# Kernel tuning notes

Measured on AMD Instinct MI355X. Metric: run time of the kernel, lower is better.

The kernel has to match this reference:

```python
import jax, jax.numpy as jnp
import numpy as np

DELTA_BEARING = 30.0
DELTA_HEADING = 30.0
N_HEAD = int(360 / DELTA_HEADING)  # 12
N_BEAR = int(360 / DELTA_BEARING)  # 12
B, P, D = 512, 128, 64
EPS = 1e-5


def setup_inputs() -> dict:
    key = jax.random.key(0)
    ks = jax.random.split(key, 8)
    hidden_state = jax.random.normal(ks[0], (B, P, D), dtype=jnp.float32)
    distance_matrix = jax.random.uniform(ks[1], (B, P, P), dtype=jnp.float32) * 10.0
    bearing_matrix = jax.random.uniform(ks[2], (B, P, P), dtype=jnp.float32) * 360.0
    heading_matrix = jax.random.uniform(ks[3], (B, P, P), dtype=jnp.float32) * 360.0
    sequence_mask = (jax.random.uniform(ks[4], (B, P)) < 0.8).astype(jnp.float32)
    domain = jax.random.normal(ks[5], (N_HEAD, N_BEAR), dtype=jnp.float32) * 2.0 + 5.0
    W = jax.random.normal(ks[6], (D, 2 * D), dtype=jnp.float32) / np.sqrt(2 * D)
    b = jnp.zeros((D,), dtype=jnp.float32)
    return {"hidden_state": hidden_state, "distance_matrix": distance_matrix,
            "bearing_matrix": bearing_matrix, "heading_matrix": heading_matrix,
            "sequence_mask": sequence_mask, "domain": domain, "W": W, "b": b}


def reference(hidden_state, distance_matrix, bearing_matrix, heading_matrix,
              sequence_mask, domain, W, b):
    # discretized relative-pose lookup indices
    idx1 = jnp.clip(jnp.floor(heading_matrix / DELTA_HEADING), 0, N_HEAD - 1).astype(jnp.int32)
    idx2 = jnp.clip(jnp.floor(bearing_matrix / DELTA_BEARING), 0, N_BEAR - 1).astype(jnp.int32)
    # gather from learned domain table, subtract distance, relu  -> [B,P,P]
    w = jax.nn.relu(domain[idx1, idx2] - distance_matrix)
    # zero the diagonal (self-interaction) and invalid pedestrian pairs
    eye = jnp.eye(P, dtype=bool)
    pair_mask = sequence_mask[:, :, None] * sequence_mask[:, None, :]  # [B,P,P]
    w = jnp.where(eye[None, :, :], 0.0, w)
    w = jnp.where(pair_mask != 0, w, 0.0)
    # masked softmax over dim=2: mask = (w != 0)
    mask = (w != 0).astype(w.dtype)
    masked_exps = jnp.exp(w) * mask + EPS
    weights = masked_exps / (masked_exps.sum(axis=2, keepdims=True) + EPS)
    # aggregate neighbor hidden states and fuse
    weighted_hidden = jnp.einsum('bpq,bqd->bpd', weights, hidden_state)
    fused = jnp.concatenate([weighted_hidden, hidden_state], axis=2)  # [B,P,2D]
    out = jnp.tanh(fused @ W.T + b)
    return out
```

## Files before the change

kernel.cpp:

```cpp
#include <hip/hip_runtime.h>
#include <hip/hip_bf16.h>
#include <math.h>

#define NB 512
#define NP 128
#define ND 64
#define EPSF 1e-5f
#define SW 136

typedef __attribute__((ext_vector_type(8))) short short8;
typedef __attribute__((ext_vector_type(4))) float f32x4;

__device__ __forceinline__ short f2bf(float x) {
    __hip_bfloat16 h = __float2bfloat16(x);
    return *reinterpret_cast<short*>(&h);
}

__global__ __launch_bounds__(256, 2) void spatial_attn_kernel(
    const float* __restrict__ hidden,
    const float* __restrict__ dist,
    const float* __restrict__ bear,
    const float* __restrict__ head,
    const float* __restrict__ smask,
    const float* __restrict__ domain,
    const float* __restrict__ W,
    const float* __restrict__ bias,
    float* __restrict__ out)
{
    __shared__ __align__(16) short s_w[NP * SW];
    __shared__ __align__(16) short s_hT[ND * SW];
    __shared__ __align__(16) short s_Wm[ND * SW];
    __shared__ float s_dom[144];
    __shared__ float s_mask[NP];

    const int b    = blockIdx.x;
    const int tid  = threadIdx.x;
    const int lane = tid & 63;
    const int wave = tid >> 6;
    const int quad = lane >> 4;
    const int l16  = lane & 15;

    {
        const float4* hsrc = (const float4*)(hidden + (size_t)b * NP * ND);
        #pragma unroll
        for (int i = 0; i < 8; ++i) {
            int idx = tid + i * 256;
            float4 v = hsrc[idx];
            int q = idx >> 4;
            int d = (idx & 15) * 4;
            s_hT[(d + 0) * SW + q] = f2bf(v.x);
            s_hT[(d + 1) * SW + q] = f2bf(v.y);
            s_hT[(d + 2) * SW + q] = f2bf(v.z);
            s_hT[(d + 3) * SW + q] = f2bf(v.w);
        }
    }
    {
        #pragma unroll
        for (int i = 0; i < 8; ++i) {
            int idx = tid + i * 256;
            float4 v = ((const float4*)W)[idx];
            int d = idx >> 5;
            int k = (idx & 31) * 4;
            short4 s4;
            s4.x = f2bf(v.x); s4.y = f2bf(v.y); s4.z = f2bf(v.z); s4.w = f2bf(v.w);
            *(short4*)&s_Wm[d * SW + k] = s4;
        }
    }
    if (tid < 144) s_dom[tid] = domain[tid];
    if (tid < NP)  s_mask[tid] = smask[b * NP + tid];
    __syncthreads();

    const int R0 = wave * 32;
    const size_t rowbase = (size_t)b * NP * NP;
    const float mq0 = s_mask[lane], mq1 = s_mask[lane + 64];

    for (int j = 0; j < 8; ++j) {
        #pragma unroll
        for (int r = 0; r < 4; ++r) {
            const int p = R0 + j * 4 + r;
            const size_t ro = rowbase + (size_t)p * NP;
            float dq0 = dist[ro + lane], dq1 = dist[ro + lane + 64];
            float bq0 = bear[ro + lane], bq1 = bear[ro + lane + 64];
            float hq0 = head[ro + lane], hq1 = head[ro + lane + 64];
            const float mp = s_mask[p];

            int i1 = (int)floorf(hq0 / 30.0f); i1 = i1 < 0 ? 0 : (i1 > 11 ? 11 : i1);
            int i2 = (int)floorf(bq0 / 30.0f); i2 = i2 < 0 ? 0 : (i2 > 11 ? 11 : i2);
            float wv0 = s_dom[i1 * 12 + i2] - dq0;
            bool on0 = (wv0 > 0.0f) && (mp != 0.0f) && (mq0 != 0.0f) && (lane != p);
            float e0 = on0 ? (expf(wv0) + EPSF) : EPSF;

            int k1 = (int)floorf(hq1 / 30.0f); k1 = k1 < 0 ? 0 : (k1 > 11 ? 11 : k1);
            int k2 = (int)floorf(bq1 / 30.0f); k2 = k2 < 0 ? 0 : (k2 > 11 ? 11 : k2);
            float wv1 = s_dom[k1 * 12 + k2] - dq1;
            bool on1 = (wv1 > 0.0f) && (mp != 0.0f) && (mq1 != 0.0f) && ((lane + 64) != p);
            float e1 = on1 ? (expf(wv1) + EPSF) : EPSF;

            float ssum = e0 + e1;
            #pragma unroll
            for (int off = 32; off > 0; off >>= 1)
                ssum += __shfl_xor(ssum, off, 64);
            float inv = 1.0f / (ssum + EPSF);
            s_w[p * SW + lane]      = f2bf(e0 * inv);
            s_w[p * SW + lane + 64] = f2bf(e1 * inv);
        }
    }

    f32x4 acc[2][4];
    #pragma unroll
    for (int ti = 0; ti < 2; ++ti)
        #pragma unroll
        for (int tj = 0; tj < 4; ++tj)
            acc[ti][tj] = (f32x4){0.f, 0.f, 0.f, 0.f};

    #pragma unroll
    for (int kb = 0; kb < 4; ++kb) {
        const int ko = kb * 32 + quad * 8;
        short8 a0 = *(const short8*)&s_w[(R0 + l16) * SW + ko];
        short8 a1 = *(const short8*)&s_w[(R0 + 16 + l16) * SW + ko];
        #pragma unroll
        for (int tj = 0; tj < 4; ++tj) {
            short8 bf = *(const short8*)&s_hT[(tj * 16 + l16) * SW + ko];
            acc[0][tj] = __builtin_amdgcn_mfma_f32_16x16x32_bf16(a0, bf, acc[0][tj], 0, 0, 0);
            acc[1][tj] = __builtin_amdgcn_mfma_f32_16x16x32_bf16(a1, bf, acc[1][tj], 0, 0, 0);
        }
    }

    #pragma unroll
    for (int ti = 0; ti < 2; ++ti)
        #pragma unroll
        for (int tj = 0; tj < 4; ++tj)
            #pragma unroll
            for (int r = 0; r < 4; ++r) {
                int row = R0 + ti * 16 + quad * 4 + r;
                s_w[row * SW + tj * 16 + l16] = f2bf(acc[ti][tj][r]);
            }
    {
        const float* hb = hidden + (size_t)b * NP * ND;
        #pragma unroll 4
        for (int i = 0; i < 32; ++i) {
            float hv = hb[(size_t)(R0 + i) * ND + lane];
            s_w[(R0 + i) * SW + 64 + lane] = f2bf(hv);
        }
    }

    f32x4 acc2[2][4];
    #pragma unroll
    for (int ti = 0; ti < 2; ++ti)
        #pragma unroll
        for (int tj = 0; tj < 4; ++tj)
            acc2[ti][tj] = (f32x4){0.f, 0.f, 0.f, 0.f};

    #pragma unroll
    for (int kb = 0; kb < 4; ++kb) {
        const int ko = kb * 32 + quad * 8;
        short8 a0 = *(const short8*)&s_w[(R0 + l16) * SW + ko];
        short8 a1 = *(const short8*)&s_w[(R0 + 16 + l16) * SW + ko];
        #pragma unroll
        for (int tj = 0; tj < 4; ++tj) {
            short8 bf = *(const short8*)&s_Wm[(tj * 16 + l16) * SW + ko];
            acc2[0][tj] = __builtin_amdgcn_mfma_f32_16x16x32_bf16(a0, bf, acc2[0][tj], 0, 0, 0);
            acc2[1][tj] = __builtin_amdgcn_mfma_f32_16x16x32_bf16(a1, bf, acc2[1][tj], 0, 0, 0);
        }
    }

    float bvals[4];
    #pragma unroll
    for (int tj = 0; tj < 4; ++tj) bvals[tj] = bias[tj * 16 + l16];

    float* ob = out + (size_t)b * NP * ND;
    #pragma unroll
    for (int ti = 0; ti < 2; ++ti)
        #pragma unroll
        for (int tj = 0; tj < 4; ++tj)
            #pragma unroll
            for (int r = 0; r < 4; ++r) {
                int row = R0 + ti * 16 + quad * 4 + r;
                ob[(size_t)row * ND + tj * 16 + l16] = tanhf(acc2[ti][tj][r] + bvals[tj]);
            }
}

extern "C" void kernel_launch(void* const* d_in, const int* in_sizes, int n_in,
                              void* d_out, int out_size, void* d_ws, size_t ws_size,
                              hipStream_t stream) {
    const float* hidden = (const float*)d_in[0];
    const float* dist   = (const float*)d_in[1];
    const float* bear   = (const float*)d_in[2];
    const float* head   = (const float*)d_in[3];
    const float* smask  = (const float*)d_in[4];
    const float* domain = (const float*)d_in[5];
    const float* W      = (const float*)d_in[6];
    const float* bias   = (const float*)d_in[7];
    float* out = (float*)d_out;

    spatial_attn_kernel<<<dim3(NB), dim3(256), 0, stream>>>(
        hidden, dist, bear, head, smask, domain, W, bias, out);
}
```

Measured before the change: 156.7 us.

## Split fused kernel into parallel weights kernel and MFMA fuse kernel via workspace

```diff
diff --git a/kernel.cpp b/kernel.cpp
--- a/kernel.cpp
+++ b/kernel.cpp
@@ -16,15 +16,185 @@
     return *reinterpret_cast<short*>(&h);
 }
 
-__global__ __launch_bounds__(256, 2) void spatial_attn_kernel(
-    const float* __restrict__ hidden,
+__global__ __launch_bounds__(256, 4) void weights_kernel(
     const float* __restrict__ dist,
     const float* __restrict__ bear,
     const float* __restrict__ head,
     const float* __restrict__ smask,
     const float* __restrict__ domain,
+    short* __restrict__ wout)
+{
+    __shared__ float s_dom[144];
+    __shared__ float s_mask[NP];
+
+    const int blk  = blockIdx.x;
+    const int b    = blk >> 5;
+    const int p0   = (blk & 31) * 4;
+    const int tid  = threadIdx.x;
+    const int lane = tid & 63;
+    const int wave = tid >> 6;
+
+    if (tid < 144) s_dom[tid] = domain[tid];
+    if (tid < NP)  s_mask[tid] = smask[b * NP + tid];
+    __syncthreads();
+
+    const int p = p0 + wave;
+    const size_t ro = ((size_t)b * NP + p) * NP;
+
+    float dq0 = dist[ro + lane], dq1 = dist[ro + lane + 64];
+    float bq0 = bear[ro + lane], bq1 = bear[ro + lane + 64];
+    float hq0 = head[ro + lane], hq1 = head[ro + lane + 64];
+    const float mp  = s_mask[p];
+    const float mq0 = s_mask[lane], mq1 = s_mask[lane + 64];
+
+    int i1 = (int)floorf(hq0 / 30.0f); i1 = i1 < 0 ? 0 : (i1 > 11 ? 11 : i1);
+    int i2 = (int)floorf(bq0 / 30.0f); i2 = i2 < 0 ? 0 : (i2 > 11 ? 11 : i2);
+    float wv0 = s_dom[i1 * 12 + i2] - dq0;
+    bool on0 = (wv0 > 0.0f) && (mp != 0.0f) && (mq0 != 0.0f) && (lane != p);
+    float e0 = on0 ? (expf(wv0) + EPSF) : EPSF;
+
+    int k1 = (int)floorf(hq1 / 30.0f); k1 = k1 < 0 ? 0 : (k1 > 11 ? 11 : k1);
+    int k2 = (int)floorf(bq1 / 30.0f); k2 = k2 < 0 ? 0 : (k2 > 11 ? 11 : k2);
+    float wv1 = s_dom[k1 * 12 + k2] - dq1;
+    bool on1 = (wv1 > 0.0f) && (mp != 0.0f) && (mq1 != 0.0f) && ((lane + 64) != p);
+    float e1 = on1 ? (expf(wv1) + EPSF) : EPSF;
+
+    float ssum = e0 + e1;
+    #pragma unroll
+    for (int off = 32; off > 0; off >>= 1)
+        ssum += __shfl_xor(ssum, off, 64);
+    float inv = 1.0f / (ssum + EPSF);
+
+    wout[ro + lane]      = f2bf(e0 * inv);
+    wout[ro + lane + 64] = f2bf(e1 * inv);
+}
+
+__global__ __launch_bounds__(256, 3) void fuse_kernel(
+    const short* __restrict__ win,
+    const float* __restrict__ hidden,
     const float* __restrict__ W,
     const float* __restrict__ bias,
+    float* __restrict__ out)
+{
+    __shared__ __align__(16) short s_w[64 * SW];
+    __shared__ __align__(16) short s_hT[ND * SW];
+    __shared__ __align__(16) short s_Wm[ND * SW];
+
+    const int blk  = blockIdx.x;
+    const int b    = blk >> 1;
+    const int half = blk & 1;
+    const int tid  = threadIdx.x;
+    const int lane = tid & 63;
+    const int wave = tid >> 6;
+    const int quad = lane >> 4;
+    const int l16  = lane & 15;
+
+    {
+        const short8* wsrc = (const short8*)(win + ((size_t)b * NP + half * 64) * NP);
+        #pragma unroll
+        for (int i = 0; i < 4; ++i) {
+            int idx = tid + i * 256;
+            int row = idx >> 4;
+            int col = (idx & 15) * 8;
+            *(short8*)&s_w[row * SW + col] = wsrc[idx];
+        }
+    }
+    {
+        const float4* hsrc = (const float4*)(hidden + (size_t)b * NP * ND);
+        #pragma unroll
+        for (int i = 0; i < 8; ++i) {
+            int idx = tid + i * 256;
+            float4 v = hsrc[idx];
+            int q = idx >> 4;
+            int d = (idx & 15) * 4;
+            s_hT[(d + 0) * SW + q] = f2bf(v.x);
+            s_hT[(d + 1) * SW + q] = f2bf(v.y);
+            s_hT[(d + 2) * SW + q] = f2bf(v.z);
+            s_hT[(d + 3) * SW + q] = f2bf(v.w);
+        }
+    }
+    {
+        #pragma unroll
+        for (int i = 0; i < 8; ++i) {
+            int idx = tid + i * 256;
+            float4 v = ((const float4*)W)[idx];
+            int d = idx >> 5;
+            int k = (idx & 31) * 4;
+            short4 s4;
+            s4.x = f2bf(v.x); s4.y = f2bf(v.y); s4.z = f2bf(v.z); s4.w = f2bf(v.w);
+            *(short4*)&s_Wm[d * SW + k] = s4;
+        }
+    }
+    __syncthreads();
+
+    const int R0 = wave * 16;
+    const int G0 = half * 64 + R0;
+
+    f32x4 acc[4];
+    #pragma unroll
+    for (int tj = 0; tj < 4; ++tj) acc[tj] = (f32x4){0.f, 0.f, 0.f, 0.f};
+
+    #pragma unroll
+    for (int kb = 0; kb < 4; ++kb) {
+        const int ko = kb * 32 + quad * 8;
+        short8 a = *(const short8*)&s_w[(R0 + l16) * SW + ko];
+        #pragma unroll
+        for (int tj = 0; tj < 4; ++tj) {
+            short8 bf = *(const short8*)&s_hT[(tj * 16 + l16) * SW + ko];
+            acc[tj] = __builtin_amdgcn_mfma_f32_16x16x32_bf16(a, bf, acc[tj], 0, 0, 0);
+        }
+    }
+
+    #pragma unroll
+    for (int tj = 0; tj < 4; ++tj)
+        #pragma unroll
+        for (int r = 0; r < 4; ++r) {
+            int row = R0 + quad * 4 + r;
+            s_w[row * SW + tj * 16 + l16] = f2bf(acc[tj][r]);
+        }
+    {
+        const float* hb = hidden + (size_t)b * NP * ND;
+        #pragma unroll 4
+        for (int i = 0; i < 16; ++i) {
+            float hv = hb[(size_t)(G0 + i) * ND + lane];
+            s_w[(R0 + i) * SW + 64 + lane] = f2bf(hv);
+        }
+    }
+
+    f32x4 acc2[4];
+    #pragma unroll
+    for (int tj = 0; tj < 4; ++tj) acc2[tj] = (f32x4){0.f, 0.f, 0.f, 0.f};
+
+    #pragma unroll
+    for (int kb = 0; kb < 4; ++kb) {
+        const int ko = kb * 32 + quad * 8;
+        short8 a = *(const short8*)&s_w[(R0 + l16) * SW + ko];
+        #pragma unroll
+        for (int tj = 0; tj < 4; ++tj) {
+            short8 bf = *(const short8*)&s_Wm[(tj * 16 + l16) * SW + ko];
+            acc2[tj] = __builtin_amdgcn_mfma_f32_16x16x32_bf16(a, bf, acc2[tj], 0, 0, 0);
+        }
+    }
+
+    float bvals[4];
+    #pragma unroll
+    for (int tj = 0; tj < 4; ++tj) bvals[tj] = bias[tj * 16 + l16];
+
+    float* ob = out + (size_t)b * NP * ND;
+    #pragma unroll
+    for (int tj = 0; tj < 4; ++tj)
+        #pragma unroll
+        for (int r = 0; r < 4; ++r) {
+            int row = G0 + quad * 4 + r;
+            ob[(size_t)row * ND + tj * 16 + l16] = tanhf(acc2[tj][r] + bvals[tj]);
+        }
+}
+
+__global__ __launch_bounds__(256, 2) void spatial_attn_single(
+    const float* __restrict__ hidden, const float* __restrict__ dist,
+    const float* __restrict__ bear, const float* __restrict__ head,
+    const float* __restrict__ smask, const float* __restrict__ domain,
+    const float* __restrict__ W, const float* __restrict__ bias,
     float* __restrict__ out)
 {
     __shared__ __align__(16) short s_w[NP * SW];
@@ -33,12 +203,8 @@
     __shared__ float s_dom[144];
     __shared__ float s_mask[NP];
 
-    const int b    = blockIdx.x;
-    const int tid  = threadIdx.x;
-    const int lane = tid & 63;
-    const int wave = tid >> 6;
-    const int quad = lane >> 4;
-    const int l16  = lane & 15;
+    const int b = blockIdx.x, tid = threadIdx.x;
+    const int lane = tid & 63, wave = tid >> 6, quad = lane >> 4, l16 = lane & 15;
 
     {
         const float4* hsrc = (const float4*)(hidden + (size_t)b * NP * ND);
@@ -46,21 +212,17 @@
         for (int i = 0; i < 8; ++i) {
             int idx = tid + i * 256;
             float4 v = hsrc[idx];
-            int q = idx >> 4;
-            int d = (idx & 15) * 4;
+            int q = idx >> 4, d = (idx & 15) * 4;
             s_hT[(d + 0) * SW + q] = f2bf(v.x);
             s_hT[(d + 1) * SW + q] = f2bf(v.y);
             s_hT[(d + 2) * SW + q] = f2bf(v.z);
             s_hT[(d + 3) * SW + q] = f2bf(v.w);
         }
-    }
-    {
         #pragma unroll
         for (int i = 0; i < 8; ++i) {
             int idx = tid + i * 256;
             float4 v = ((const float4*)W)[idx];
-            int d = idx >> 5;
-            int k = (idx & 31) * 4;
+            int d = idx >> 5, k = (idx & 31) * 4;
             short4 s4;
             s4.x = f2bf(v.x); s4.y = f2bf(v.y); s4.z = f2bf(v.z); s4.w = f2bf(v.w);
             *(short4*)&s_Wm[d * SW + k] = s4;
@@ -83,19 +245,16 @@
             float bq0 = bear[ro + lane], bq1 = bear[ro + lane + 64];
             float hq0 = head[ro + lane], hq1 = head[ro + lane + 64];
             const float mp = s_mask[p];
-
             int i1 = (int)floorf(hq0 / 30.0f); i1 = i1 < 0 ? 0 : (i1 > 11 ? 11 : i1);
             int i2 = (int)floorf(bq0 / 30.0f); i2 = i2 < 0 ? 0 : (i2 > 11 ? 11 : i2);
             float wv0 = s_dom[i1 * 12 + i2] - dq0;
             bool on0 = (wv0 > 0.0f) && (mp != 0.0f) && (mq0 != 0.0f) && (lane != p);
             float e0 = on0 ? (expf(wv0) + EPSF) : EPSF;
-
             int k1 = (int)floorf(hq1 / 30.0f); k1 = k1 < 0 ? 0 : (k1 > 11 ? 11 : k1);
             int k2 = (int)floorf(bq1 / 30.0f); k2 = k2 < 0 ? 0 : (k2 > 11 ? 11 : k2);
             float wv1 = s_dom[k1 * 12 + k2] - dq1;
             bool on1 = (wv1 > 0.0f) && (mp != 0.0f) && (mq1 != 0.0f) && ((lane + 64) != p);
             float e1 = on1 ? (expf(wv1) + EPSF) : EPSF;
-
             float ssum = e0 + e1;
             #pragma unroll
             for (int off = 32; off > 0; off >>= 1)
@@ -110,9 +269,7 @@
     #pragma unroll
     for (int ti = 0; ti < 2; ++ti)
         #pragma unroll
-        for (int tj = 0; tj < 4; ++tj)
-            acc[ti][tj] = (f32x4){0.f, 0.f, 0.f, 0.f};
-
+        for (int tj = 0; tj < 4; ++tj) acc[ti][tj] = (f32x4){0.f, 0.f, 0.f, 0.f};
     #pragma unroll
     for (int kb = 0; kb < 4; ++kb) {
         const int ko = kb * 32 + quad * 8;
@@ -125,7 +282,6 @@
             acc[1][tj] = __builtin_amdgcn_mfma_f32_16x16x32_bf16(a1, bf, acc[1][tj], 0, 0, 0);
         }
     }
-
     #pragma unroll
     for (int ti = 0; ti < 2; ++ti)
         #pragma unroll
@@ -143,14 +299,11 @@
             s_w[(R0 + i) * SW + 64 + lane] = f2bf(hv);
         }
     }
-
     f32x4 acc2[2][4];
     #pragma unroll
     for (int ti = 0; ti < 2; ++ti)
         #pragma unroll
-        for (int tj = 0; tj < 4; ++tj)
-            acc2[ti][tj] = (f32x4){0.f, 0.f, 0.f, 0.f};
-
+        for (int tj = 0; tj < 4; ++tj) acc2[ti][tj] = (f32x4){0.f, 0.f, 0.f, 0.f};
     #pragma unroll
     for (int kb = 0; kb < 4; ++kb) {
         const int ko = kb * 32 + quad * 8;
@@ -163,11 +316,9 @@
             acc2[1][tj] = __builtin_amdgcn_mfma_f32_16x16x32_bf16(a1, bf, acc2[1][tj], 0, 0, 0);
         }
     }
-
     float bvals[4];
     #pragma unroll
     for (int tj = 0; tj < 4; ++tj) bvals[tj] = bias[tj * 16 + l16];
-
     float* ob = out + (size_t)b * NP * ND;
     #pragma unroll
     for (int ti = 0; ti < 2; ++ti)
@@ -193,6 +344,15 @@
     const float* bias   = (const float*)d_in[7];
     float* out = (float*)d_out;
 
-    spatial_attn_kernel<<<dim3(NB), dim3(256), 0, stream>>>(
-        hidden, dist, bear, head, smask, domain, W, bias, out);
-}
+    const size_t need = (size_t)NB * NP * NP * sizeof(short);
+    if (ws_size >= need) {
+        short* wbuf = (short*)d_ws;
+        weights_kernel<<<dim3(NB * 32), dim3(256), 0, stream>>>(
+            dist, bear, head, smask, domain, wbuf);
+        fuse_kernel<<<dim3(NB * 2), dim3(256), 0, stream>>>(
+            wbuf, hidden, W, bias, out);
+    } else {
+        spatial_attn_single<<<dim3(NB), dim3(256), 0, stream>>>(
+            hidden, dist, bear, head, smask, domain, W, bias, out);
+    }
+}
```

Measured after the change: 163.9 us. +4.6%, slower.

## Use 8 waves per block and defer softmax normalization to MFMA rowsum

Applied to the files above, without the earlier changes.

```diff
diff --git a/kernel.cpp b/kernel.cpp
--- a/kernel.cpp
+++ b/kernel.cpp
@@ -16,7 +16,7 @@
     return *reinterpret_cast<short*>(&h);
 }
 
-__global__ __launch_bounds__(256, 2) void spatial_attn_kernel(
+__global__ __launch_bounds__(512, 4) void spatial_attn_kernel(
     const float* __restrict__ hidden,
     const float* __restrict__ dist,
     const float* __restrict__ bear,
@@ -43,8 +43,8 @@
     {
         const float4* hsrc = (const float4*)(hidden + (size_t)b * NP * ND);
         #pragma unroll
-        for (int i = 0; i < 8; ++i) {
-            int idx = tid + i * 256;
+        for (int i = 0; i < 4; ++i) {
+            int idx = tid + i * 512;
             float4 v = hsrc[idx];
             int q = idx >> 4;
             int d = (idx & 15) * 4;
@@ -56,8 +56,8 @@
     }
     {
         #pragma unroll
-        for (int i = 0; i < 8; ++i) {
-            int idx = tid + i * 256;
+        for (int i = 0; i < 4; ++i) {
+            int idx = tid + i * 512;
             float4 v = ((const float4*)W)[idx];
             int d = idx >> 5;
             int k = (idx & 31) * 4;
@@ -70,14 +70,14 @@
     if (tid < NP)  s_mask[tid] = smask[b * NP + tid];
     __syncthreads();
 
-    const int R0 = wave * 32;
+    const int R0 = wave * 16;
     const size_t rowbase = (size_t)b * NP * NP;
     const float mq0 = s_mask[lane], mq1 = s_mask[lane + 64];
 
-    for (int j = 0; j < 8; ++j) {
+    for (int j0 = 0; j0 < 16; j0 += 4) {
         #pragma unroll
         for (int r = 0; r < 4; ++r) {
-            const int p = R0 + j * 4 + r;
+            const int p = R0 + j0 + r;
             const size_t ro = rowbase + (size_t)p * NP;
             float dq0 = dist[ro + lane], dq1 = dist[ro + lane + 64];
             float bq0 = bear[ro + lane], bq1 = bear[ro + lane + 64];
@@ -96,71 +96,64 @@
             bool on1 = (wv1 > 0.0f) && (mp != 0.0f) && (mq1 != 0.0f) && ((lane + 64) != p);
             float e1 = on1 ? (expf(wv1) + EPSF) : EPSF;
 
-            float ssum = e0 + e1;
-            #pragma unroll
-            for (int off = 32; off > 0; off >>= 1)
-                ssum += __shfl_xor(ssum, off, 64);
-            float inv = 1.0f / (ssum + EPSF);
-            s_w[p * SW + lane]      = f2bf(e0 * inv);
-            s_w[p * SW + lane + 64] = f2bf(e1 * inv);
+            s_w[p * SW + lane]      = f2bf(e0);
+            s_w[p * SW + lane + 64] = f2bf(e1);
         }
     }
 
-    f32x4 acc[2][4];
+    f32x4 acc[4], accs;
     #pragma unroll
-    for (int ti = 0; ti < 2; ++ti)
-        #pragma unroll
-        for (int tj = 0; tj < 4; ++tj)
-            acc[ti][tj] = (f32x4){0.f, 0.f, 0.f, 0.f};
+    for (int tj = 0; tj < 4; ++tj) acc[tj] = (f32x4){0.f, 0.f, 0.f, 0.f};
+    accs = (f32x4){0.f, 0.f, 0.f, 0.f};
+
+    short8 ones;
+    #pragma unroll
+    for (int i = 0; i < 8; ++i) ones[i] = (short)0x3F80;
 
     #pragma unroll
     for (int kb = 0; kb < 4; ++kb) {
         const int ko = kb * 32 + quad * 8;
-        short8 a0 = *(const short8*)&s_w[(R0 + l16) * SW + ko];
-        short8 a1 = *(const short8*)&s_w[(R0 + 16 + l16) * SW + ko];
+        short8 a = *(const short8*)&s_w[(R0 + l16) * SW + ko];
+        accs = __builtin_amdgcn_mfma_f32_16x16x32_bf16(a, ones, accs, 0, 0, 0);
         #pragma unroll
         for (int tj = 0; tj < 4; ++tj) {
             short8 bf = *(const short8*)&s_hT[(tj * 16 + l16) * SW + ko];
-            acc[0][tj] = __builtin_amdgcn_mfma_f32_16x16x32_bf16(a0, bf, acc[0][tj], 0, 0, 0);
-            acc[1][tj] = __builtin_amdgcn_mfma_f32_16x16x32_bf16(a1, bf, acc[1][tj], 0, 0, 0);
+            acc[tj] = __builtin_amdgcn_mfma_f32_16x16x32_bf16(a, bf, acc[tj], 0, 0, 0);
         }
     }
 
+    float inv[4];
     #pragma unroll
-    for (int ti = 0; ti < 2; ++ti)
+    for (int r = 0; r < 4; ++r) inv[r] = 1.0f / (accs[r] + EPSF);
+
+    #pragma unroll
+    for (int tj = 0; tj < 4; ++tj)
         #pragma unroll
-        for (int tj = 0; tj < 4; ++tj)
-            #pragma unroll
-            for (int r = 0; r < 4; ++r) {
-                int row = R0 + ti * 16 + quad * 4 + r;
-                s_w[row * SW + tj * 16 + l16] = f2bf(acc[ti][tj][r]);
-            }
+        for (int r = 0; r < 4; ++r) {
+            int row = R0 + quad * 4 + r;
+            s_w[row * SW + tj * 16 + l16] = f2bf(acc[tj][r] * inv[r]);
+        }
     {
         const float* hb = hidden + (size_t)b * NP * ND;
         #pragma unroll 4
-        for (int i = 0; i < 32; ++i) {
+        for (int i = 0; i < 16; ++i) {
             float hv = hb[(size_t)(R0 + i) * ND + lane];
             s_w[(R0 + i) * SW + 64 + lane] = f2bf(hv);
         }
     }
 
-    f32x4 acc2[2][4];
+    f32x4 acc2[4];
     #pragma unroll
-    for (int ti = 0; ti < 2; ++ti)
-        #pragma unroll
-        for (int tj = 0; tj < 4; ++tj)
-            acc2[ti][tj] = (f32x4){0.f, 0.f, 0.f, 0.f};
+    for (int tj = 0; tj < 4; ++tj) acc2[tj] = (f32x4){0.f, 0.f, 0.f, 0.f};
 
     #pragma unroll
     for (int kb = 0; kb < 4; ++kb) {
         const int ko = kb * 32 + quad * 8;
-        short8 a0 = *(const short8*)&s_w[(R0 + l16) * SW + ko];
-        short8 a1 = *(const short8*)&s_w[(R0 + 16 + l16) * SW + ko];
+        short8 a = *(const short8*)&s_w[(R0 + l16) * SW + ko];
         #pragma unroll
         for (int tj = 0; tj < 4; ++tj) {
             short8 bf = *(const short8*)&s_Wm[(tj * 16 + l16) * SW + ko];
-            acc2[0][tj] = __builtin_amdgcn_mfma_f32_16x16x32_bf16(a0, bf, acc2[0][tj], 0, 0, 0);
-            acc2[1][tj] = __builtin_amdgcn_mfma_f32_16x16x32_bf16(a1, bf, acc2[1][tj], 0, 0, 0);
+            acc2[tj] = __builtin_amdgcn_mfma_f32_16x16x32_bf16(a, bf, acc2[tj], 0, 0, 0);
         }
     }
 
@@ -170,14 +163,12 @@
 
     float* ob = out + (size_t)b * NP * ND;
     #pragma unroll
-    for (int ti = 0; ti < 2; ++ti)
+    for (int tj = 0; tj < 4; ++tj)
         #pragma unroll
-        for (int tj = 0; tj < 4; ++tj)
-            #pragma unroll
-            for (int r = 0; r < 4; ++r) {
-                int row = R0 + ti * 16 + quad * 4 + r;
-                ob[(size_t)row * ND + tj * 16 + l16] = tanhf(acc2[ti][tj][r] + bvals[tj]);
-            }
+        for (int r = 0; r < 4; ++r) {
+            int row = R0 + quad * 4 + r;
+            ob[(size_t)row * ND + tj * 16 + l16] = tanhf(acc2[tj][r] + bvals[tj]);
+        }
 }
 
 extern "C" void kernel_launch(void* const* d_in, const int* in_sizes, int n_in,
@@ -193,6 +184,6 @@
     const float* bias   = (const float*)d_in[7];
     float* out = (float*)d_out;
 
-    spatial_attn_kernel<<<dim3(NB), dim3(256), 0, stream>>>(
+    spatial_attn_kernel<<<dim3(NB), dim3(512), 0, stream>>>(
         hidden, dist, bear, head, smask, domain, W, bias, out);
 }
```

New measurement: 157.2 us. About the same (+0.4%).
